# Performance work log

Measured on AMD Instinct MI355X. Metric: run time of the kernel, lower is better.

The kernel has to match this reference:

```python
import jax, jax.numpy as jnp
import numpy as np

N = 50000   # num nodes
E = 800000  # num edges (avg degree 16)
D = 128     # in = hidden = out channels


def setup_inputs() -> dict:
    key = jax.random.key(0)
    k0, k1, k2, k3, k4, k5 = jax.random.split(key, 6)
    x = jax.random.normal(k0, (N, D), dtype=jnp.float32)
    edge_index = jax.random.randint(k1, (2, E), 0, N, dtype=jnp.int32)
    scale = 1.0 / np.sqrt(D)
    W1 = jax.random.normal(k2, (D, D), dtype=jnp.float32) * scale
    b1 = jax.random.normal(k3, (D,), dtype=jnp.float32) * 0.01
    W2 = jax.random.normal(k4, (D, D), dtype=jnp.float32) * scale
    b2 = jax.random.normal(k5, (D,), dtype=jnp.float32) * 0.01
    return {"x": x, "edge_index": edge_index, "W1": W1, "b1": b1, "W2": W2, "b2": b2}


def reference(x, edge_index, W1, b1, W2, b2):
    n = x.shape[0]
    src, dst = edge_index[0], edge_index[1]
    # GCN adds self-loops before normalization
    loops = jnp.arange(n, dtype=src.dtype)
    s = jnp.concatenate([src, loops])
    d = jnp.concatenate([dst, loops])
    # symmetric normalization: deg^{-1/2}[s] * deg^{-1/2}[d]
    deg = jax.ops.segment_sum(jnp.ones_like(d, dtype=x.dtype), d, num_segments=n)
    dinv = jnp.where(deg > 0, jax.lax.rsqrt(deg), 0.0)
    ew = dinv[s] * dinv[d]  # [E+N]

    def gcn_conv(h, W, b):
        h = h @ W                                   # [N, D] dense transform first
        msg = ew[:, None] * h[s]                     # gather over edges [E+N, D]
        agg = jax.ops.segment_sum(msg, d, num_segments=n)  # scatter-add [N, D]
        return agg + b

    # layer 1: conv -> Identity BN -> ELU (dropout=0.0 -> no-op)
    h = jax.nn.elu(gcn_conv(x, W1, b1))
    # layer 2 (last): conv -> Identity BN -> ELU
    out = jax.nn.elu(gcn_conv(h, W2, b2))
    return out
```

## Files before the change

kernel.cpp:

```cpp
#include <hip/hip_runtime.h>
#include <math.h>

#define D 128
#define BCAP 8192
#define SLICE 64
#define PB 256

typedef __attribute__((ext_vector_type(8))) short bf16x8;
typedef __attribute__((ext_vector_type(4))) float f32x4;


__device__ inline float2 bf2f2(unsigned int u) {
    union { unsigned int i; float f; } a, b;
    a.i = u << 16;
    b.i = u & 0xffff0000u;
    return make_float2(a.f, b.f);
}

__device__ inline unsigned short f2bf(float f) {
    union { float f; unsigned int i; } u;
    u.f = f;
    unsigned int r = u.i + 0x7fffu + ((u.i >> 16) & 1u);
    return (unsigned short)(r >> 16);
}


__device__ __forceinline__ void gemm_core(unsigned short (*Ws)[136], int gbid,
                                          const void* __restrict__ Ain, int a_fp32,
                                          unsigned int* __restrict__ Cb, int N) {
    const int tid = threadIdx.x;
    const int wid = tid >> 6;
    const int lane = tid & 63;
    const int quad = lane >> 4;
    const int ln = lane & 15;
    const int m = gbid * 64 + wid * 16 + ln;
    const bool valid = (m < N);

    f32x4 acc[8];
#pragma unroll
    for (int c = 0; c < 8; ++c) acc[c] = (f32x4){0.f, 0.f, 0.f, 0.f};

    __syncthreads();

#pragma unroll
    for (int ks = 0; ks < 4; ++ks) {
        const int k0 = ks * 32;
        bf16x8 af;
        if (a_fp32) {
            const float* A = (const float*)Ain;
            float4 lo = make_float4(0.f, 0.f, 0.f, 0.f), hi = lo;
            if (valid) {
                lo = *(const float4*)&A[(size_t)m * 128 + k0 + quad * 8];
                hi = *(const float4*)&A[(size_t)m * 128 + k0 + quad * 8 + 4];
            }
            af[0] = (short)f2bf(lo.x); af[1] = (short)f2bf(lo.y);
            af[2] = (short)f2bf(lo.z); af[3] = (short)f2bf(lo.w);
            af[4] = (short)f2bf(hi.x); af[5] = (short)f2bf(hi.y);
            af[6] = (short)f2bf(hi.z); af[7] = (short)f2bf(hi.w);
        } else {
            const uint4* A4 = (const uint4*)Ain;
            uint4 v = valid ? A4[(size_t)m * 16 + ks * 4 + quad]
                            : make_uint4(0u, 0u, 0u, 0u);
            union { uint4 u; bf16x8 h; } cv;
            cv.u = v;
            af = cv.h;
        }
#pragma unroll
        for (int c = 0; c < 8; ++c) {
            bf16x8 bf = *(const bf16x8*)&Ws[c * 16 + ln][k0 + quad * 8];
            acc[c] = __builtin_amdgcn_mfma_f32_16x16x32_bf16(af, bf, acc[c], 0, 0, 0);
        }
    }

    const int rowbase = gbid * 64 + wid * 16 + quad * 4;
#pragma unroll
    for (int c = 0; c < 8; ++c) {
#pragma unroll
        for (int r = 0; r < 4; ++r) {
            float v = acc[c][r];
            float vn = __shfl_xor(v, 1);
            int grow = rowbase + r;
            if (!(ln & 1) && grow < N) {
                unsigned int u = (unsigned int)f2bf(v) | ((unsigned int)f2bf(vn) << 16);
                Cb[(size_t)grow * 64 + c * 8 + (ln >> 1)] = u;
            }
        }
    }
}


__global__ __launch_bounds__(256) void k1_all(
        const int* __restrict__ src, const int* __restrict__ dst,
        const float* __restrict__ x, const float* __restrict__ W1,
        const float* __restrict__ W2, unsigned short* __restrict__ Wt2,
        unsigned int* __restrict__ pairs, unsigned char* __restrict__ cellCnt,
        unsigned int* __restrict__ hb1, int e, int chunk, int N, int gemmBlocks) {
    __shared__ __align__(16) unsigned char smem[128 * 136 * 2];
    const int tid = threadIdx.x;
    const int bid = blockIdx.x;

    if (bid < PB) {
        int* cur = (int*)smem;
        cur[tid] = 0;
        __syncthreads();
        const int e0 = bid * chunk;
        const int e1 = min(e0 + chunk, e);
        for (int i = e0 + tid; i < e1; i += 256) {
            int d = dst[i], s = src[i];
            int b = d >> 8;
            int off = atomicAdd(&cur[b], 1);
            if (off < SLICE)
                pairs[((size_t)(bid * 256 + b)) * SLICE + off] =
                    (unsigned int)s | ((unsigned int)(d & 255) << 16);
        }
        __syncthreads();
        cellCnt[bid * 256 + tid] = (unsigned char)min(cur[tid], SLICE);
    } else if (bid < PB + gemmBlocks) {
        unsigned short (*Ws)[136] = (unsigned short(*)[136])smem;
        for (int j = 0; j < 64; ++j) {
            int idx = tid + j * 256;
            Ws[idx & 127][idx >> 7] = f2bf(W1[idx]);
        }
        gemm_core(Ws, bid - PB, x, 1, hb1, N);
    } else {
        int i = (bid - PB - gemmBlocks) * 256 + tid;
        int k = i >> 7, n = i & 127;
        Wt2[n * 128 + k] = f2bf(W2[i]);
    }
}


__global__ __launch_bounds__(256) void partB(const unsigned int* __restrict__ pairs,
                                             const unsigned char* __restrict__ cellCnt,
                                             unsigned short* __restrict__ col,
                                             unsigned int* __restrict__ meta,
                                             float* __restrict__ dinv, int n) {
    __shared__ int deg[256];
    __shared__ int sc[256];
    __shared__ int cur[256];
    const int b = blockIdx.x;
    const int tid = threadIdx.x;

    deg[tid] = 0;
    __syncthreads();

    const int c = cellCnt[tid * 256 + b];
    const unsigned int* cell = pairs + ((size_t)(tid * 256 + b)) * SLICE;
    for (int q = 0; q < c; ++q) atomicAdd(&deg[cell[q] >> 16], 1);
    __syncthreads();

    int v = deg[tid];
    sc[tid] = v;
    __syncthreads();
    for (int o = 1; o < 256; o <<= 1) {
        int t = (tid >= o) ? sc[tid - o] : 0;
        __syncthreads();
        sc[tid] += t;
        __syncthreads();
    }
    int startw = sc[tid] - v;
    cur[tid] = startw;

    int node = b * 256 + tid;
    if (node < n) {
        meta[node] = ((unsigned int)(b * BCAP + startw) << 10) | (unsigned int)v;
        dinv[node] = rsqrtf((float)(v + 1));
    }
    __syncthreads();

    for (int q = 0; q < c; ++q) {
        unsigned int p = cell[q];
        int dl = p >> 16;
        int off = atomicAdd(&cur[dl], 1);
        col[(size_t)b * BCAP + off] = (unsigned short)(p & 0xffffu);
    }
}


__device__ __forceinline__ float2 agg_node(const unsigned int* __restrict__ hb,
                                           const unsigned short* __restrict__ col,
                                           const float* __restrict__ dinv,
                                           int node, int lane, float2 bv,
                                           unsigned int m, float di) {
    float2 self = bf2f2(hb[(size_t)node * 64 + lane]);
    float2 a0 = make_float2(di * self.x, di * self.y);
    float2 a1 = make_float2(0.f, 0.f), a2 = make_float2(0.f, 0.f),
           a3 = make_float2(0.f, 0.f), a4 = make_float2(0.f, 0.f),
           a5 = make_float2(0.f, 0.f), a6 = make_float2(0.f, 0.f),
           a7 = make_float2(0.f, 0.f);

    const int s0 = (int)(m >> 10);
    const int s1 = s0 + (int)(m & 1023u);
    int i = s0;
    for (; i + 8 <= s1; i += 8) {
        int c0 = col[i + 0], c1 = col[i + 1], c2 = col[i + 2], c3 = col[i + 3];
        int c4 = col[i + 4], c5 = col[i + 5], c6 = col[i + 6], c7 = col[i + 7];
        float w0 = dinv[c0], w1 = dinv[c1], w2 = dinv[c2], w3 = dinv[c3];
        float w4 = dinv[c4], w5 = dinv[c5], w6 = dinv[c6], w7 = dinv[c7];
        unsigned int u0 = hb[(size_t)c0 * 64 + lane];
        unsigned int u1 = hb[(size_t)c1 * 64 + lane];
        unsigned int u2 = hb[(size_t)c2 * 64 + lane];
        unsigned int u3 = hb[(size_t)c3 * 64 + lane];
        unsigned int u4 = hb[(size_t)c4 * 64 + lane];
        unsigned int u5 = hb[(size_t)c5 * 64 + lane];
        unsigned int u6 = hb[(size_t)c6 * 64 + lane];
        unsigned int u7 = hb[(size_t)c7 * 64 + lane];
        float2 v0 = bf2f2(u0), v1 = bf2f2(u1), v2 = bf2f2(u2), v3 = bf2f2(u3);
        float2 v4 = bf2f2(u4), v5 = bf2f2(u5), v6 = bf2f2(u6), v7 = bf2f2(u7);
        a0.x = fmaf(w0, v0.x, a0.x); a0.y = fmaf(w0, v0.y, a0.y);
        a1.x = fmaf(w1, v1.x, a1.x); a1.y = fmaf(w1, v1.y, a1.y);
        a2.x = fmaf(w2, v2.x, a2.x); a2.y = fmaf(w2, v2.y, a2.y);
        a3.x = fmaf(w3, v3.x, a3.x); a3.y = fmaf(w3, v3.y, a3.y);
        a4.x = fmaf(w4, v4.x, a4.x); a4.y = fmaf(w4, v4.y, a4.y);
        a5.x = fmaf(w5, v5.x, a5.x); a5.y = fmaf(w5, v5.y, a5.y);
        a6.x = fmaf(w6, v6.x, a6.x); a6.y = fmaf(w6, v6.y, a6.y);
        a7.x = fmaf(w7, v7.x, a7.x); a7.y = fmaf(w7, v7.y, a7.y);
    }
    for (; i < s1; ++i) {
        int c = col[i];
        float ww = dinv[c];
        float2 v = bf2f2(hb[(size_t)c * 64 + lane]);
        a0.x = fmaf(ww, v.x, a0.x); a0.y = fmaf(ww, v.y, a0.y);
    }

    float sx = (a0.x + a1.x) + (a2.x + a3.x) + (a4.x + a5.x) + (a6.x + a7.x);
    float sy = (a0.y + a1.y) + (a2.y + a3.y) + (a4.y + a5.y) + (a6.y + a7.y);
    float rx = fmaf(di, sx, bv.x);
    float ry = fmaf(di, sy, bv.y);
    rx = rx > 0.0f ? rx : expm1f(rx);
    ry = ry > 0.0f ? ry : expm1f(ry);
    return make_float2(rx, ry);
}


__global__ __launch_bounds__(1024, 8) void k3_agg_gemm(
        const unsigned int* __restrict__ hb1, const unsigned int* __restrict__ meta,
        const unsigned short* __restrict__ col, const float* __restrict__ dinv,
        const float* __restrict__ b1, const unsigned short* __restrict__ Wt2,
        unsigned int* __restrict__ hb2, int n) {
    __shared__ unsigned int g1s[16 * 68];
    __shared__ __align__(16) unsigned short Ws[128][136];

    const int tid = threadIdx.x;
    const int wid = tid >> 6;
    const int lane = tid & 63;
    const int nodeBase = blockIdx.x * 16;
    const int node = nodeBase + wid;

    {
        const int nloc = tid >> 3;
        const int kb = (tid & 7) * 16;
        const uint4* g = (const uint4*)(Wt2 + (size_t)nloc * 128 + kb);
        uint4* s = (uint4*)&Ws[nloc][kb];
        s[0] = g[0];
        s[1] = g[1];
    }

    const float2 bv = ((const float2*)b1)[lane];
    unsigned int packed = 0;
    if (node < n) {
        const unsigned int m = meta[node];
        const float di = dinv[node];
        float2 r = agg_node(hb1, col, dinv, node, lane, bv, m, di);
        packed = (unsigned int)f2bf(r.x) | ((unsigned int)f2bf(r.y) << 16);
    }
    g1s[wid * 68 + lane] = packed;
    __syncthreads();

    if (wid < 8) {
        const int quad = lane >> 4;
        const int ln = lane & 15;
        f32x4 acc = (f32x4){0.f, 0.f, 0.f, 0.f};
#pragma unroll
        for (int ks = 0; ks < 4; ++ks) {
            bf16x8 af = *(const bf16x8*)&g1s[ln * 68 + ks * 16 + quad * 4];
            bf16x8 bf = *(const bf16x8*)&Ws[wid * 16 + ln][ks * 32 + quad * 8];
            acc = __builtin_amdgcn_mfma_f32_16x16x32_bf16(af, bf, acc, 0, 0, 0);
        }
#pragma unroll
        for (int r = 0; r < 4; ++r) {
            float v = acc[r];
            float vn = __shfl_xor(v, 1);
            int grow = nodeBase + quad * 4 + r;
            if (!(ln & 1) && grow < n) {
                hb2[(size_t)grow * 64 + wid * 8 + (ln >> 1)] =
                    (unsigned int)f2bf(v) | ((unsigned int)f2bf(vn) << 16);
            }
        }
    }
}


__global__ __launch_bounds__(256) void agg_elu(const unsigned int* __restrict__ hb,
                                               const unsigned int* __restrict__ meta,
                                               const unsigned short* __restrict__ col,
                                               const float* __restrict__ dinv,
                                               const float* __restrict__ bias,
                                               float* __restrict__ outf, int n) {
    const int wid = threadIdx.x >> 6;
    const int lane = threadIdx.x & 63;
    const int node = blockIdx.x * 4 + wid;
    if (node >= n) return;
    const float2 bv = ((const float2*)bias)[lane];
    const unsigned int m = meta[node];
    const float di = dinv[node];
    float2 r = agg_node(hb, col, dinv, node, lane, bv, m, di);
    ((float2*)outf)[(size_t)node * 64 + lane] = r;
}


extern "C" void kernel_launch(void* const* d_in, const int* in_sizes, int n_in,
                              void* d_out, int out_size, void* d_ws, size_t ws_size,
                              hipStream_t stream) {
    const float* x  = (const float*)d_in[0];
    const int*   ei = (const int*)d_in[1];
    const float* W1 = (const float*)d_in[2];
    const float* b1 = (const float*)d_in[3];
    const float* W2 = (const float*)d_in[4];
    const float* b2 = (const float*)d_in[5];
    float* out = (float*)d_out;

    const int N = in_sizes[0] / D;
    const int E = in_sizes[1] / 2;
    const int* src = ei;
    const int* dst = ei + E;
    const int NB = (N + 255) / 256;

    char* ws = (char*)d_ws;
    size_t off = 0;
    auto alloc = [&](size_t bytes) -> void* {
        void* p = ws + off;
        off = (off + bytes + 255) & ~(size_t)255;
        return p;
    };
    unsigned int*   pairs   = (unsigned int*)alloc((size_t)PB * 256 * SLICE * 4);
    unsigned char*  cellCnt = (unsigned char*)alloc((size_t)PB * 256);
    unsigned short* col     = (unsigned short*)alloc((size_t)NB * BCAP * 2);
    unsigned int*   meta    = (unsigned int*)alloc((size_t)N * 4);
    float*          dinv    = (float*)alloc((size_t)N * 4);
    unsigned short* Wt2     = (unsigned short*)alloc(128 * 128 * 2);
    unsigned int*   hb1     = (unsigned int*)alloc((size_t)N * 64 * 4);
    unsigned int*   hb2     = (unsigned int*)alloc((size_t)N * 64 * 4);
    (void)ws_size; (void)n_in; (void)out_size;

    const int chunk = (E + PB - 1) / PB;
    const int gemmBlocks = (N + 63) / 64;

    k1_all<<<PB + gemmBlocks + 64, 256, 0, stream>>>(src, dst, x, W1, W2, Wt2,
                                                     pairs, cellCnt, hb1, E, chunk,
                                                     N, gemmBlocks);
    partB<<<NB, 256, 0, stream>>>(pairs, cellCnt, col, meta, dinv, N);
    k3_agg_gemm<<<(N + 15) / 16, 1024, 0, stream>>>(hb1, meta, col, dinv, b1, Wt2, hb2, N);
    agg_elu<<<(N + 3) / 4, 256, 0, stream>>>(hb2, meta, col, dinv, b2, out, N);
}
```

Before: 201.5 us.

## Split aggregation into feature-slice blocks and unfuse layer-2 GEMM

Replaces the fused aggregate+GEMM kernel and the per-node aggregation kernel with an agg_slice kernel. Each wave handles one node's 32-feature slice, with four lane groups processing different edges and reducing through shuffles. The layer-1 result is written to a reused workspace buffer, and a separate gemm2 kernel applies W2. The aim is more parallelism and memory-level parallelism per gathered row, at the cost of an extra kernel launch, a global round trip for the intermediate, and four times as many block-level reads of meta and col.

```diff
diff --git a/kernel.cpp b/kernel.cpp
--- a/kernel.cpp
+++ b/kernel.cpp
@@ -177,135 +177,92 @@
 }
 
 
-__device__ __forceinline__ float2 agg_node(const unsigned int* __restrict__ hb,
-                                           const unsigned short* __restrict__ col,
-                                           const float* __restrict__ dinv,
-                                           int node, int lane, float2 bv,
-                                           unsigned int m, float di) {
-    float2 self = bf2f2(hb[(size_t)node * 64 + lane]);
-    float2 a0 = make_float2(di * self.x, di * self.y);
-    float2 a1 = make_float2(0.f, 0.f), a2 = make_float2(0.f, 0.f),
-           a3 = make_float2(0.f, 0.f), a4 = make_float2(0.f, 0.f),
-           a5 = make_float2(0.f, 0.f), a6 = make_float2(0.f, 0.f),
-           a7 = make_float2(0.f, 0.f);
-
+__global__ __launch_bounds__(256) void agg_slice(
+        const unsigned int* __restrict__ hb, const unsigned int* __restrict__ meta,
+        const unsigned short* __restrict__ col, const float* __restrict__ dinv,
+        const float* __restrict__ bias, unsigned int* __restrict__ outb,
+        float* __restrict__ outf, int n) {
+    const int bid = blockIdx.x;
+    const int s = bid & 3;
+    const int k = bid >> 2;
+    const int wid = threadIdx.x >> 6;
+    const int lane = threadIdx.x & 63;
+    const int g = lane >> 4;
+    const int ln = lane & 15;
+    const int node = k * 4 + wid;
+    if (node >= n) return;
+
+    const unsigned int m = meta[node];
+    const float di = dinv[node];
     const int s0 = (int)(m >> 10);
     const int s1 = s0 + (int)(m & 1023u);
+    const int base = s * 16 + ln;
+
+    float2 acc;
+    {
+        float2 self = bf2f2(hb[(size_t)node * 64 + base]);
+        float ws = (g == 0) ? di : 0.f;
+        acc = make_float2(ws * self.x, ws * self.y);
+    }
+    float2 acc2 = make_float2(0.f, 0.f);
+
     int i = s0;
     for (; i + 8 <= s1; i += 8) {
-        int c0 = col[i + 0], c1 = col[i + 1], c2 = col[i + 2], c3 = col[i + 3];
-        int c4 = col[i + 4], c5 = col[i + 5], c6 = col[i + 6], c7 = col[i + 7];
-        float w0 = dinv[c0], w1 = dinv[c1], w2 = dinv[c2], w3 = dinv[c3];
-        float w4 = dinv[c4], w5 = dinv[c5], w6 = dinv[c6], w7 = dinv[c7];
-        unsigned int u0 = hb[(size_t)c0 * 64 + lane];
-        unsigned int u1 = hb[(size_t)c1 * 64 + lane];
-        unsigned int u2 = hb[(size_t)c2 * 64 + lane];
-        unsigned int u3 = hb[(size_t)c3 * 64 + lane];
-        unsigned int u4 = hb[(size_t)c4 * 64 + lane];
-        unsigned int u5 = hb[(size_t)c5 * 64 + lane];
-        unsigned int u6 = hb[(size_t)c6 * 64 + lane];
-        unsigned int u7 = hb[(size_t)c7 * 64 + lane];
-        float2 v0 = bf2f2(u0), v1 = bf2f2(u1), v2 = bf2f2(u2), v3 = bf2f2(u3);
-        float2 v4 = bf2f2(u4), v5 = bf2f2(u5), v6 = bf2f2(u6), v7 = bf2f2(u7);
-        a0.x = fmaf(w0, v0.x, a0.x); a0.y = fmaf(w0, v0.y, a0.y);
-        a1.x = fmaf(w1, v1.x, a1.x); a1.y = fmaf(w1, v1.y, a1.y);
-        a2.x = fmaf(w2, v2.x, a2.x); a2.y = fmaf(w2, v2.y, a2.y);
-        a3.x = fmaf(w3, v3.x, a3.x); a3.y = fmaf(w3, v3.y, a3.y);
-        a4.x = fmaf(w4, v4.x, a4.x); a4.y = fmaf(w4, v4.y, a4.y);
-        a5.x = fmaf(w5, v5.x, a5.x); a5.y = fmaf(w5, v5.y, a5.y);
-        a6.x = fmaf(w6, v6.x, a6.x); a6.y = fmaf(w6, v6.y, a6.y);
-        a7.x = fmaf(w7, v7.x, a7.x); a7.y = fmaf(w7, v7.y, a7.y);
-    }
-    for (; i < s1; ++i) {
-        int c = col[i];
-        float ww = dinv[c];
-        float2 v = bf2f2(hb[(size_t)c * 64 + lane]);
-        a0.x = fmaf(ww, v.x, a0.x); a0.y = fmaf(ww, v.y, a0.y);
-    }
-
-    float sx = (a0.x + a1.x) + (a2.x + a3.x) + (a4.x + a5.x) + (a6.x + a7.x);
-    float sy = (a0.y + a1.y) + (a2.y + a3.y) + (a4.y + a5.y) + (a6.y + a7.y);
-    float rx = fmaf(di, sx, bv.x);
-    float ry = fmaf(di, sy, bv.y);
-    rx = rx > 0.0f ? rx : expm1f(rx);
-    ry = ry > 0.0f ? ry : expm1f(ry);
-    return make_float2(rx, ry);
-}
-
-
-__global__ __launch_bounds__(1024, 8) void k3_agg_gemm(
-        const unsigned int* __restrict__ hb1, const unsigned int* __restrict__ meta,
-        const unsigned short* __restrict__ col, const float* __restrict__ dinv,
-        const float* __restrict__ b1, const unsigned short* __restrict__ Wt2,
-        unsigned int* __restrict__ hb2, int n) {
-    __shared__ unsigned int g1s[16 * 68];
+        int ca = col[i + g];
+        int cb = col[i + 4 + g];
+        float wa = dinv[ca], wb = dinv[cb];
+        unsigned int ua = hb[(size_t)ca * 64 + base];
+        unsigned int ub = hb[(size_t)cb * 64 + base];
+        float2 va = bf2f2(ua), vb = bf2f2(ub);
+        acc.x  = fmaf(wa, va.x, acc.x);  acc.y  = fmaf(wa, va.y, acc.y);
+        acc2.x = fmaf(wb, vb.x, acc2.x); acc2.y = fmaf(wb, vb.y, acc2.y);
+    }
+    for (; i < s1; i += 4) {
+        if (i + g < s1) {
+            int c = col[i + g];
+            float w = dinv[c];
+            float2 v = bf2f2(hb[(size_t)c * 64 + base]);
+            acc.x = fmaf(w, v.x, acc.x);
+            acc.y = fmaf(w, v.y, acc.y);
+        }
+    }
+    acc.x += acc2.x;
+    acc.y += acc2.y;
+
+    acc.x += __shfl_xor(acc.x, 16);
+    acc.y += __shfl_xor(acc.y, 16);
+    acc.x += __shfl_xor(acc.x, 32);
+    acc.y += __shfl_xor(acc.y, 32);
+
+    if (g == 0) {
+        const float2 bv = ((const float2*)bias)[base];
+        float rx = fmaf(di, acc.x, bv.x);
+        float ry = fmaf(di, acc.y, bv.y);
+        rx = rx > 0.0f ? rx : expm1f(rx);
+        ry = ry > 0.0f ? ry : expm1f(ry);
+        if (outb) {
+            outb[(size_t)node * 64 + base] =
+                (unsigned int)f2bf(rx) | ((unsigned int)f2bf(ry) << 16);
+        } else {
+            ((float2*)outf)[(size_t)node * 64 + base] = make_float2(rx, ry);
+        }
+    }
+}
+
+
+__global__ __launch_bounds__(256) void gemm2(const unsigned short* __restrict__ Wt2,
+                                             const unsigned int* __restrict__ g1,
+                                             unsigned int* __restrict__ hb2, int N) {
     __shared__ __align__(16) unsigned short Ws[128][136];
-
     const int tid = threadIdx.x;
-    const int wid = tid >> 6;
-    const int lane = tid & 63;
-    const int nodeBase = blockIdx.x * 16;
-    const int node = nodeBase + wid;
-
-    {
-        const int nloc = tid >> 3;
-        const int kb = (tid & 7) * 16;
-        const uint4* g = (const uint4*)(Wt2 + (size_t)nloc * 128 + kb);
-        uint4* s = (uint4*)&Ws[nloc][kb];
-        s[0] = g[0];
-        s[1] = g[1];
-    }
-
-    const float2 bv = ((const float2*)b1)[lane];
-    unsigned int packed = 0;
-    if (node < n) {
-        const unsigned int m = meta[node];
-        const float di = dinv[node];
-        float2 r = agg_node(hb1, col, dinv, node, lane, bv, m, di);
-        packed = (unsigned int)f2bf(r.x) | ((unsigned int)f2bf(r.y) << 16);
-    }
-    g1s[wid * 68 + lane] = packed;
-    __syncthreads();
-
-    if (wid < 8) {
-        const int quad = lane >> 4;
-        const int ln = lane & 15;
-        f32x4 acc = (f32x4){0.f, 0.f, 0.f, 0.f};
-#pragma unroll
-        for (int ks = 0; ks < 4; ++ks) {
-            bf16x8 af = *(const bf16x8*)&g1s[ln * 68 + ks * 16 + quad * 4];
-            bf16x8 bf = *(const bf16x8*)&Ws[wid * 16 + ln][ks * 32 + quad * 8];
-            acc = __builtin_amdgcn_mfma_f32_16x16x32_bf16(af, bf, acc, 0, 0, 0);
-        }
-#pragma unroll
-        for (int r = 0; r < 4; ++r) {
-            float v = acc[r];
-            float vn = __shfl_xor(v, 1);
-            int grow = nodeBase + quad * 4 + r;
-            if (!(ln & 1) && grow < n) {
-                hb2[(size_t)grow * 64 + wid * 8 + (ln >> 1)] =
-                    (unsigned int)f2bf(v) | ((unsigned int)f2bf(vn) << 16);
-            }
-        }
-    }
-}
-
-
-__global__ __launch_bounds__(256) void agg_elu(const unsigned int* __restrict__ hb,
-                                               const unsigned int* __restrict__ meta,
-                                               const unsigned short* __restrict__ col,
-                                               const float* __restrict__ dinv,
-                                               const float* __restrict__ bias,
-                                               float* __restrict__ outf, int n) {
-    const int wid = threadIdx.x >> 6;
-    const int lane = threadIdx.x & 63;
-    const int node = blockIdx.x * 4 + wid;
-    if (node >= n) return;
-    const float2 bv = ((const float2*)bias)[lane];
-    const unsigned int m = meta[node];
-    const float di = dinv[node];
-    float2 r = agg_node(hb, col, dinv, node, lane, bv, m, di);
-    ((float2*)outf)[(size_t)node * 64 + lane] = r;
+#pragma unroll
+    for (int j = 0; j < 16; ++j) {
+        int q = tid + j * 256;
+        int r = q >> 4;
+        int cidx = q & 15;
+        *(uint4*)&Ws[r][cidx * 8] = ((const uint4*)Wt2)[q];
+    }
+    gemm_core(Ws, blockIdx.x, g1, 0, hb2, N);
 }
 
 
@@ -341,15 +298,20 @@
     unsigned short* Wt2     = (unsigned short*)alloc(128 * 128 * 2);
     unsigned int*   hb1     = (unsigned int*)alloc((size_t)N * 64 * 4);
     unsigned int*   hb2     = (unsigned int*)alloc((size_t)N * 64 * 4);
+    unsigned int*   g1      = pairs;
     (void)ws_size; (void)n_in; (void)out_size;
 
     const int chunk = (E + PB - 1) / PB;
     const int gemmBlocks = (N + 63) / 64;
+    const int nodeQuads = (N + 3) / 4;
 
     k1_all<<<PB + gemmBlocks + 64, 256, 0, stream>>>(src, dst, x, W1, W2, Wt2,
                                                      pairs, cellCnt, hb1, E, chunk,
                                                      N, gemmBlocks);
     partB<<<NB, 256, 0, stream>>>(pairs, cellCnt, col, meta, dinv, N);
-    k3_agg_gemm<<<(N + 15) / 16, 1024, 0, stream>>>(hb1, meta, col, dinv, b1, Wt2, hb2, N);
-    agg_elu<<<(N + 3) / 4, 256, 0, stream>>>(hb2, meta, col, dinv, b2, out, N);
-}
+    agg_slice<<<nodeQuads * 4, 256, 0, stream>>>(hb1, meta, col, dinv, b1,
+                                                 g1, nullptr, N);
+    gemm2<<<gemmBlocks, 256, 0, stream>>>(Wt2, g1, hb2, N);
+    agg_slice<<<nodeQuads * 4, 256, 0, stream>>>(hb2, meta, col, dinv, b2,
+                                                 nullptr, out, N);
+}
```

Result: slower. 289.3 us (+43.6%).

## Split each wave into four edge groups with 16-byte row gathers

Applied to the files above, without the earlier changes.

Aggregation now splits each wave into four 16-lane groups. Each lane loads a 16-byte vector covering 8 bf16 features, so one wave gathers four neighbor rows at once. Partial sums are then combined across groups with xor shuffles. This replaces the old scheme, where each lane loaded 4 bytes of one neighbor row per iteration, and aims for wider memory transactions and more rows in flight per wave. The tail iterations pad with zero-weight self loads, which adds shuffle work and wasted loads on low-degree nodes. Launch-bound occupancy hints are also changed.

```diff
diff --git a/kernel.cpp b/kernel.cpp
--- a/kernel.cpp
+++ b/kernel.cpp
@@ -8,6 +8,7 @@
 
 typedef __attribute__((ext_vector_type(8))) short bf16x8;
 typedef __attribute__((ext_vector_type(4))) float f32x4;
+typedef __attribute__((ext_vector_type(4))) unsigned int u32x4;
 
 
 __device__ inline float2 bf2f2(unsigned int u) {
@@ -177,63 +178,67 @@
 }
 
 
-__device__ __forceinline__ float2 agg_node(const unsigned int* __restrict__ hb,
-                                           const unsigned short* __restrict__ col,
-                                           const float* __restrict__ dinv,
-                                           int node, int lane, float2 bv,
-                                           unsigned int m, float di) {
-    float2 self = bf2f2(hb[(size_t)node * 64 + lane]);
-    float2 a0 = make_float2(di * self.x, di * self.y);
-    float2 a1 = make_float2(0.f, 0.f), a2 = make_float2(0.f, 0.f),
-           a3 = make_float2(0.f, 0.f), a4 = make_float2(0.f, 0.f),
-           a5 = make_float2(0.f, 0.f), a6 = make_float2(0.f, 0.f),
-           a7 = make_float2(0.f, 0.f);
-
+__device__ __forceinline__ void fma8(float w, u32x4 u, f32x4& a, f32x4& b) {
+    float2 v0 = bf2f2(u.x), v1 = bf2f2(u.y), v2 = bf2f2(u.z), v3 = bf2f2(u.w);
+    a[0] = fmaf(w, v0.x, a[0]); a[1] = fmaf(w, v0.y, a[1]);
+    a[2] = fmaf(w, v1.x, a[2]); a[3] = fmaf(w, v1.y, a[3]);
+    b[0] = fmaf(w, v2.x, b[0]); b[1] = fmaf(w, v2.y, b[1]);
+    b[2] = fmaf(w, v3.x, b[2]); b[3] = fmaf(w, v3.y, b[3]);
+}
+
+__device__ __forceinline__ void agg_wave(const unsigned int* __restrict__ hb,
+                                         const unsigned short* __restrict__ col,
+                                         const float* __restrict__ dinv,
+                                         int node, int g, int ln,
+                                         unsigned int m, float di,
+                                         f32x4& sA, f32x4& sB) {
+    const u32x4* hb4 = (const u32x4*)hb;
     const int s0 = (int)(m >> 10);
     const int s1 = s0 + (int)(m & 1023u);
+
+    {
+        u32x4 su = hb4[(size_t)node * 16 + ln];
+        float ws = (g == 0) ? di : 0.f;
+        fma8(ws, su, sA, sB);
+    }
+
     int i = s0;
-    for (; i + 8 <= s1; i += 8) {
-        int c0 = col[i + 0], c1 = col[i + 1], c2 = col[i + 2], c3 = col[i + 3];
-        int c4 = col[i + 4], c5 = col[i + 5], c6 = col[i + 6], c7 = col[i + 7];
-        float w0 = dinv[c0], w1 = dinv[c1], w2 = dinv[c2], w3 = dinv[c3];
-        float w4 = dinv[c4], w5 = dinv[c5], w6 = dinv[c6], w7 = dinv[c7];
-        unsigned int u0 = hb[(size_t)c0 * 64 + lane];
-        unsigned int u1 = hb[(size_t)c1 * 64 + lane];
-        unsigned int u2 = hb[(size_t)c2 * 64 + lane];
-        unsigned int u3 = hb[(size_t)c3 * 64 + lane];
-        unsigned int u4 = hb[(size_t)c4 * 64 + lane];
-        unsigned int u5 = hb[(size_t)c5 * 64 + lane];
-        unsigned int u6 = hb[(size_t)c6 * 64 + lane];
-        unsigned int u7 = hb[(size_t)c7 * 64 + lane];
-        float2 v0 = bf2f2(u0), v1 = bf2f2(u1), v2 = bf2f2(u2), v3 = bf2f2(u3);
-        float2 v4 = bf2f2(u4), v5 = bf2f2(u5), v6 = bf2f2(u6), v7 = bf2f2(u7);
-        a0.x = fmaf(w0, v0.x, a0.x); a0.y = fmaf(w0, v0.y, a0.y);
-        a1.x = fmaf(w1, v1.x, a1.x); a1.y = fmaf(w1, v1.y, a1.y);
-        a2.x = fmaf(w2, v2.x, a2.x); a2.y = fmaf(w2, v2.y, a2.y);
-        a3.x = fmaf(w3, v3.x, a3.x); a3.y = fmaf(w3, v3.y, a3.y);
-        a4.x = fmaf(w4, v4.x, a4.x); a4.y = fmaf(w4, v4.y, a4.y);
-        a5.x = fmaf(w5, v5.x, a5.x); a5.y = fmaf(w5, v5.y, a5.y);
-        a6.x = fmaf(w6, v6.x, a6.x); a6.y = fmaf(w6, v6.y, a6.y);
-        a7.x = fmaf(w7, v7.x, a7.x); a7.y = fmaf(w7, v7.y, a7.y);
-    }
-    for (; i < s1; ++i) {
-        int c = col[i];
-        float ww = dinv[c];
-        float2 v = bf2f2(hb[(size_t)c * 64 + lane]);
-        a0.x = fmaf(ww, v.x, a0.x); a0.y = fmaf(ww, v.y, a0.y);
-    }
-
-    float sx = (a0.x + a1.x) + (a2.x + a3.x) + (a4.x + a5.x) + (a6.x + a7.x);
-    float sy = (a0.y + a1.y) + (a2.y + a3.y) + (a4.y + a5.y) + (a6.y + a7.y);
-    float rx = fmaf(di, sx, bv.x);
-    float ry = fmaf(di, sy, bv.y);
-    rx = rx > 0.0f ? rx : expm1f(rx);
-    ry = ry > 0.0f ? ry : expm1f(ry);
-    return make_float2(rx, ry);
-}
-
-
-__global__ __launch_bounds__(1024, 8) void k3_agg_gemm(
+    for (; i + 16 <= s1; i += 16) {
+        const int c0 = col[i + g];
+        const int c1 = col[i + 4 + g];
+        const int c2 = col[i + 8 + g];
+        const int c3 = col[i + 12 + g];
+        const float w0 = dinv[c0], w1 = dinv[c1], w2 = dinv[c2], w3 = dinv[c3];
+        u32x4 u0 = hb4[(size_t)c0 * 16 + ln];
+        u32x4 u1 = hb4[(size_t)c1 * 16 + ln];
+        u32x4 u2 = hb4[(size_t)c2 * 16 + ln];
+        u32x4 u3 = hb4[(size_t)c3 * 16 + ln];
+        asm volatile("" :: "v"(u0), "v"(u1), "v"(u2), "v"(u3));
+        fma8(w0, u0, sA, sB);
+        fma8(w1, u1, sA, sB);
+        fma8(w2, u2, sA, sB);
+        fma8(w3, u3, sA, sB);
+    }
+    while (i < s1) {
+        const int t = i + g;
+        const int cc = (t < s1) ? (int)col[t] : node;
+        const float w = (t < s1) ? dinv[cc] : 0.f;
+        u32x4 u = hb4[(size_t)cc * 16 + ln];
+        fma8(w, u, sA, sB);
+        i += 4;
+    }
+
+#pragma unroll
+    for (int k = 0; k < 4; ++k) {
+        sA[k] += __shfl_xor(sA[k], 16);
+        sA[k] += __shfl_xor(sA[k], 32);
+        sB[k] += __shfl_xor(sB[k], 16);
+        sB[k] += __shfl_xor(sB[k], 32);
+    }
+}
+
+
+__global__ __launch_bounds__(1024, 4) void k3_agg_gemm(
         const unsigned int* __restrict__ hb1, const unsigned int* __restrict__ meta,
         const unsigned short* __restrict__ col, const float* __restrict__ dinv,
         const float* __restrict__ b1, const unsigned short* __restrict__ Wt2,
@@ -244,32 +249,53 @@
     const int tid = threadIdx.x;
     const int wid = tid >> 6;
     const int lane = tid & 63;
+    const int g = lane >> 4;
+    const int ln = lane & 15;
     const int nodeBase = blockIdx.x * 16;
     const int node = nodeBase + wid;
 
     {
         const int nloc = tid >> 3;
         const int kb = (tid & 7) * 16;
-        const uint4* g = (const uint4*)(Wt2 + (size_t)nloc * 128 + kb);
-        uint4* s = (uint4*)&Ws[nloc][kb];
-        s[0] = g[0];
-        s[1] = g[1];
-    }
-
-    const float2 bv = ((const float2*)b1)[lane];
-    unsigned int packed = 0;
+        const uint4* gp = (const uint4*)(Wt2 + (size_t)nloc * 128 + kb);
+        uint4* sp = (uint4*)&Ws[nloc][kb];
+        sp[0] = gp[0];
+        sp[1] = gp[1];
+    }
+
+    f32x4 sA = (f32x4){0.f, 0.f, 0.f, 0.f};
+    f32x4 sB = (f32x4){0.f, 0.f, 0.f, 0.f};
     if (node < n) {
         const unsigned int m = meta[node];
         const float di = dinv[node];
-        float2 r = agg_node(hb1, col, dinv, node, lane, bv, m, di);
-        packed = (unsigned int)f2bf(r.x) | ((unsigned int)f2bf(r.y) << 16);
-    }
-    g1s[wid * 68 + lane] = packed;
+        agg_wave(hb1, col, dinv, node, g, ln, m, di, sA, sB);
+
+        const float4 bA = ((const float4*)b1)[2 * ln];
+        const float4 bB = ((const float4*)b1)[2 * ln + 1];
+        float r0 = fmaf(di, sA[0], bA.x), r1 = fmaf(di, sA[1], bA.y);
+        float r2 = fmaf(di, sA[2], bA.z), r3 = fmaf(di, sA[3], bA.w);
+        float r4 = fmaf(di, sB[0], bB.x), r5 = fmaf(di, sB[1], bB.y);
+        float r6 = fmaf(di, sB[2], bB.z), r7 = fmaf(di, sB[3], bB.w);
+        r0 = r0 > 0.f ? r0 : expm1f(r0); r1 = r1 > 0.f ? r1 : expm1f(r1);
+        r2 = r2 > 0.f ? r2 : expm1f(r2); r3 = r3 > 0.f ? r3 : expm1f(r3);
+        r4 = r4 > 0.f ? r4 : expm1f(r4); r5 = r5 > 0.f ? r5 : expm1f(r5);
+        r6 = r6 > 0.f ? r6 : expm1f(r6); r7 = r7 > 0.f ? r7 : expm1f(r7);
+        if (g == 0) {
+            g1s[wid * 68 + ln * 4 + 0] = (unsigned int)f2bf(r0) | ((unsigned int)f2bf(r1) << 16);
+            g1s[wid * 68 + ln * 4 + 1] = (unsigned int)f2bf(r2) | ((unsigned int)f2bf(r3) << 16);
+            g1s[wid * 68 + ln * 4 + 2] = (unsigned int)f2bf(r4) | ((unsigned int)f2bf(r5) << 16);
+            g1s[wid * 68 + ln * 4 + 3] = (unsigned int)f2bf(r6) | ((unsigned int)f2bf(r7) << 16);
+        }
+    } else if (g == 0) {
+        g1s[wid * 68 + ln * 4 + 0] = 0u;
+        g1s[wid * 68 + ln * 4 + 1] = 0u;
+        g1s[wid * 68 + ln * 4 + 2] = 0u;
+        g1s[wid * 68 + ln * 4 + 3] = 0u;
+    }
     __syncthreads();
 
     if (wid < 8) {
         const int quad = lane >> 4;
-        const int ln = lane & 15;
         f32x4 acc = (f32x4){0.f, 0.f, 0.f, 0.f};
 #pragma unroll
         for (int ks = 0; ks < 4; ++ks) {
@@ -291,21 +317,44 @@
 }
 
 
-__global__ __launch_bounds__(256) void agg_elu(const unsigned int* __restrict__ hb,
-                                               const unsigned int* __restrict__ meta,
-                                               const unsigned short* __restrict__ col,
-                                               const float* __restrict__ dinv,
-                                               const float* __restrict__ bias,
-                                               float* __restrict__ outf, int n) {
+__global__ __launch_bounds__(256, 4) void agg_elu(const unsigned int* __restrict__ hb,
+                                                  const unsigned int* __restrict__ meta,
+                                                  const unsigned short* __restrict__ col,
+                                                  const float* __restrict__ dinv,
+                                                  const float* __restrict__ bias,
+                                                  float* __restrict__ outf, int n) {
     const int wid = threadIdx.x >> 6;
     const int lane = threadIdx.x & 63;
+    const int g = lane >> 4;
+    const int ln = lane & 15;
     const int node = blockIdx.x * 4 + wid;
     if (node >= n) return;
-    const float2 bv = ((const float2*)bias)[lane];
+
     const unsigned int m = meta[node];
     const float di = dinv[node];
-    float2 r = agg_node(hb, col, dinv, node, lane, bv, m, di);
-    ((float2*)outf)[(size_t)node * 64 + lane] = r;
+    f32x4 sA = (f32x4){0.f, 0.f, 0.f, 0.f};
+    f32x4 sB = (f32x4){0.f, 0.f, 0.f, 0.f};
+    agg_wave(hb, col, dinv, node, g, ln, m, di, sA, sB);
+
+    if (g == 0) {
+        const float4 bA = ((const float4*)bias)[2 * ln];
+        const float4 bB = ((const float4*)bias)[2 * ln + 1];
+        float4 rA, rB;
+        rA.x = fmaf(di, sA[0], bA.x); rA.y = fmaf(di, sA[1], bA.y);
+        rA.z = fmaf(di, sA[2], bA.z); rA.w = fmaf(di, sA[3], bA.w);
+        rB.x = fmaf(di, sB[0], bB.x); rB.y = fmaf(di, sB[1], bB.y);
+        rB.z = fmaf(di, sB[2], bB.z); rB.w = fmaf(di, sB[3], bB.w);
+        rA.x = rA.x > 0.f ? rA.x : expm1f(rA.x);
+        rA.y = rA.y > 0.f ? rA.y : expm1f(rA.y);
+        rA.z = rA.z > 0.f ? rA.z : expm1f(rA.z);
+        rA.w = rA.w > 0.f ? rA.w : expm1f(rA.w);
+        rB.x = rB.x > 0.f ? rB.x : expm1f(rB.x);
+        rB.y = rB.y > 0.f ? rB.y : expm1f(rB.y);
+        rB.z = rB.z > 0.f ? rB.z : expm1f(rB.z);
+        rB.w = rB.w > 0.f ? rB.w : expm1f(rB.w);
+        ((float4*)outf)[(size_t)node * 32 + 2 * ln] = rA;
+        ((float4*)outf)[(size_t)node * 32 + 2 * ln + 1] = rB;
+    }
 }
 
 
```

Result: faster. 191.7 us (-4.9%).
